# Kernel tuning notes

Hardware: AMD Instinct MI355X
Metric: run time of the kernel (lower is better)

Reference implementation:

```python
import jax, jax.numpy as jnp
import numpy as np

DIM = 512
DEPTH = 6
HEADS = 8
HD = DIM // HEADS          # head dim = 64
HALF = HD // 4             # rope half_dim = 16
MLP_H = int(DIM * 4.0)
TOKENS = [1, 4, 16, 64]    # CLS, S1, S2, S3
N = sum(TOKENS)            # 85
MAX_FREQ = 10.0
BATCH = 1024
LN_EPS = 1e-5


def _build_mask():
    # CLS sees CLS+S3; each scale sees CLS+itself (block-diagonal + CLS column)
    m = np.full((N, N), -np.inf, dtype=np.float32)
    cum = np.cumsum([0] + TOKENS)  # [0,1,5,21,85]
    m[0, 0] = 0.0
    m[0, cum[3]:cum[4]] = 0.0
    for i in range(1, 4):
        s, e = cum[i], cum[i + 1]
        m[s:e, 0] = 0.0
        m[s:e, s:e] = 0.0
    return jnp.asarray(m)

MASK = _build_mask()
FREQS = jnp.exp(jnp.arange(HALF, dtype=jnp.float32) * (-np.log(MAX_FREQ) / HALF))


def _layer_norm(x, g, b):
    mu = x.mean(-1, keepdims=True)
    var = ((x - mu) ** 2).mean(-1, keepdims=True)
    return (x - mu) * jax.lax.rsqrt(var + LN_EPS) * g + b


def _rope2d(t, coords):
    # t: [B,H,P,HD], coords: [P,2] in [0,1]^2
    ang_x = coords[:, 0:1] * FREQS[None, :] * (2.0 * jnp.pi)  # [P,HALF]
    ang_y = coords[:, 1:2] * FREQS[None, :] * (2.0 * jnp.pi)
    cx, sx = jnp.cos(ang_x), jnp.sin(ang_x)
    cy, sy = jnp.cos(ang_y), jnp.sin(ang_y)
    B, H, P, _ = t.shape
    t = t.reshape(B, H, P, 4, HALF)
    x0, x1, x2, x3 = t[..., 0, :], t[..., 1, :], t[..., 2, :], t[..., 3, :]
    r = jnp.stack([x0 * cx - x1 * sx,
                   x0 * sx + x1 * cx,
                   x2 * cy - x3 * sy,
                   x2 * sy + x3 * cy], axis=3)
    return r.reshape(B, H, P, HD)


def _rope_skip_cls(t, coords):
    return jnp.concatenate([t[:, :, :1], _rope2d(t[:, :, 1:], coords)], axis=2)


def _block(x, coords, p):
    (ln1g, ln1b, qkvw, qkvb, projw, projb,
     ln2g, ln2b, f1w, f1b, f2w, f2b) = p
    B, Nn, D = x.shape
    h = _layer_norm(x, ln1g, ln1b)
    qkv = h @ qkvw + qkvb                         # [B,N,3D]
    qkv = qkv.reshape(B, Nn, 3, HEADS, HD).transpose(2, 0, 3, 1, 4)
    q, k, v = qkv[0], qkv[1], qkv[2]              # [B,H,N,HD]
    q = _rope_skip_cls(q, coords)
    k = _rope_skip_cls(k, coords)
    attn = jnp.einsum('bhqd,bhkd->bhqk', q, k) * (HD ** -0.5) + MASK
    attn = jax.nn.softmax(attn, axis=-1)
    out = jnp.einsum('bhqk,bhkd->bhqd', attn, v)
    out = out.transpose(0, 2, 1, 3).reshape(B, Nn, D)
    x = x + (out @ projw + projb)
    h = _layer_norm(x, ln2g, ln2b)
    h = jax.nn.gelu(h @ f1w + f1b, approximate=False) @ f2w + f2b
    return x + h


def setup_inputs() -> dict:
    key = jax.random.key(0)
    ks = jax.random.split(key, 8)
    s = 0.02
    nrm = lambda k, shape: jax.random.normal(k, shape, jnp.float32) * s
    return dict(
        x=jax.random.normal(ks[0], (BATCH, N, DIM), jnp.float32),
        coords=jax.random.uniform(ks[1], (N - 1, 2), jnp.float32),
        ln1_g=jnp.ones((DEPTH, DIM), jnp.float32),
        ln1_b=jnp.zeros((DEPTH, DIM), jnp.float32),
        qkv_w=nrm(ks[2], (DEPTH, DIM, 3 * DIM)),
        qkv_b=jnp.zeros((DEPTH, 3 * DIM), jnp.float32),
        proj_w=nrm(ks[3], (DEPTH, DIM, DIM)),
        proj_b=jnp.zeros((DEPTH, DIM), jnp.float32),
        ln2_g=jnp.ones((DEPTH, DIM), jnp.float32),
        ln2_b=jnp.zeros((DEPTH, DIM), jnp.float32),
        fc1_w=nrm(ks[4], (DEPTH, DIM, MLP_H)),
        fc1_b=jnp.zeros((DEPTH, MLP_H), jnp.float32),
        fc2_w=nrm(ks[5], (DEPTH, MLP_H, DIM)),
        fc2_b=jnp.zeros((DEPTH, DIM), jnp.float32),
    )


def reference(x, coords, ln1_g, ln1_b, qkv_w, qkv_b, proj_w, proj_b,
              ln2_g, ln2_b, fc1_w, fc1_b, fc2_w, fc2_b):
    for i in range(DEPTH):
        x = _block(x, coords,
                   (ln1_g[i], ln1_b[i], qkv_w[i], qkv_b[i], proj_w[i], proj_b[i],
                    ln2_g[i], ln2_b[i], fc1_w[i], fc1_b[i], fc2_w[i], fc2_b[i]))
    return x
```

## Files before the change

kernel.cpp:

```cpp
#include <hip/hip_runtime.h>
#include <hip/hip_bf16.h>
#include <math.h>

#define DIMX 512
#define NTOK 85
#define BATCH 1024
#define M_ROWS (BATCH * NTOK)
#define MLP_H 2048
#define DEPTH 6

typedef __attribute__((ext_vector_type(8))) short short8;
typedef __attribute__((ext_vector_type(4))) float f32x4;

__device__ inline float bf2f(ushort u) {
    union { unsigned int i; float f; } v; v.i = ((unsigned int)u) << 16; return v.f;
}
__device__ inline ushort f2bf(float f) {
    __hip_bfloat16 h = __float2bfloat16(f);
    union { __hip_bfloat16 h; ushort u; } v; v.h = h; return v.u;
}
__device__ inline unsigned int pack2(float a, float b) {
    return (unsigned int)f2bf(a) | ((unsigned int)f2bf(b) << 16);
}
__device__ inline float gelu_fast(float v) {
    float u = 1.5957691f * fmaf(0.044715f * v, v * v, v);
    return v / (1.0f + __expf(-u));
}

__device__ inline void gload16(const ushort* g, ushort* lds) {
    __builtin_amdgcn_global_load_lds(
        (const __attribute__((address_space(1))) unsigned int*)g,
        (__attribute__((address_space(3))) unsigned int*)lds, 16, 0, 0);
}

__global__ __launch_bounds__(256) void transpose_bf16(const float* __restrict__ in,
                                                      ushort* __restrict__ out,
                                                      int K, int N) {
    __shared__ float tile[32][33];
    int n0 = blockIdx.x * 32, k0 = blockIdx.y * 32;
    int tx = threadIdx.x, ty = threadIdx.y;
    #pragma unroll
    for (int j = 0; j < 32; j += 8)
        tile[ty + j][tx] = in[(size_t)(k0 + ty + j) * N + n0 + tx];
    __syncthreads();
    #pragma unroll
    for (int j = 0; j < 32; j += 8)
        out[(size_t)(n0 + ty + j) * K + k0 + tx] = f2bf(tile[tx][ty + j]);
}

__global__ void rope_table(const float* __restrict__ coords, float* __restrict__ tab) {
    int t = blockIdx.x;
    int idx = threadIdx.x;
    float freq = expf(-(float)idx * (2.302585093f / 16.0f));
    float twopi = 6.283185307179586f;
    float ax = coords[t * 2 + 0] * freq * twopi;
    float ay = coords[t * 2 + 1] * freq * twopi;
    tab[t * 64 + idx]      = cosf(ax);
    tab[t * 64 + 16 + idx] = sinf(ax);
    tab[t * 64 + 32 + idx] = cosf(ay);
    tab[t * 64 + 48 + idx] = sinf(ay);
}

__global__ __launch_bounds__(256) void ln_kernel(const float* __restrict__ x,
                                                 const float* __restrict__ g,
                                                 const float* __restrict__ bta,
                                                 ushort* __restrict__ out) {
    int w = threadIdx.x >> 6, lane = threadIdx.x & 63;
    size_t row = (size_t)blockIdx.x * 4 + w;
    const float* xr = x + row * DIMX;
    int c = lane * 8;
    float4 v0 = *(const float4*)(xr + c);
    float4 v1 = *(const float4*)(xr + c + 4);
    float s = v0.x + v0.y + v0.z + v0.w + v1.x + v1.y + v1.z + v1.w;
    #pragma unroll
    for (int m = 32; m; m >>= 1) s += __shfl_xor(s, m);
    float mu = s * (1.0f / 512.0f);
    float d0 = v0.x - mu, d1 = v0.y - mu, d2 = v0.z - mu, d3 = v0.w - mu;
    float d4 = v1.x - mu, d5 = v1.y - mu, d6 = v1.z - mu, d7 = v1.w - mu;
    float q = d0*d0 + d1*d1 + d2*d2 + d3*d3 + d4*d4 + d5*d5 + d6*d6 + d7*d7;
    #pragma unroll
    for (int m = 32; m; m >>= 1) q += __shfl_xor(q, m);
    float rs = rsqrtf(q * (1.0f / 512.0f) + 1e-5f);
    float4 g0 = *(const float4*)(g + c), g1 = *(const float4*)(g + c + 4);
    float4 b0 = *(const float4*)(bta + c), b1 = *(const float4*)(bta + c + 4);
    uint4 o;
    o.x = pack2(d0 * rs * g0.x + b0.x, d1 * rs * g0.y + b0.y);
    o.y = pack2(d2 * rs * g0.z + b0.z, d3 * rs * g0.w + b0.w);
    o.z = pack2(d4 * rs * g1.x + b1.x, d5 * rs * g1.y + b1.y);
    o.w = pack2(d6 * rs * g1.z + b1.z, d7 * rs * g1.w + b1.w);
    *(uint4*)&out[row * DIMX + c] = o;
}

template <int EPI>
__global__ __launch_bounds__(256, 2) void gemm_wide(const ushort* __restrict__ A,
                                                    const ushort* __restrict__ Bt,
                                                    const float* __restrict__ bias,
                                                    float* __restrict__ outF,
                                                    ushort* __restrict__ outB,
                                                    int M, int N, int K,
                                                    const float* __restrict__ tab) {
    __shared__ ushort AsF[3 * 8192] __attribute__((aligned(16)));
    __shared__ ushort BsF[3 * 4096] __attribute__((aligned(16)));
    int tid = threadIdx.x;
    int w = tid >> 6, lane = tid & 63;
    int wm2 = (w >> 1) * 128;
    int wn = (w & 1) * 64;

    int nbx = gridDim.x;
    int nwg = nbx * gridDim.y;
    int orig = blockIdx.y * nbx + blockIdx.x;
    int q8 = nwg >> 3, r8 = nwg & 7;
    int xcd = orig & 7, loc = orig >> 3;
    int id = (xcd < r8) ? xcd * (q8 + 1) + loc : r8 * (q8 + 1) + (xcd - r8) * q8 + loc;
    int m0 = (id / nbx) * 256;
    int n0 = (id % nbx) * 128;

    int srow = tid >> 2;
    int scol = ((tid & 3) ^ ((srow >> 1) & 3)) * 8;
    int rA0 = m0 + srow;       if (rA0 >= M) rA0 = M - 1;
    int rA1 = m0 + 64 + srow;  if (rA1 >= M) rA1 = M - 1;
    int rA2 = m0 + 128 + srow; if (rA2 >= M) rA2 = M - 1;
    int rA3 = m0 + 192 + srow; if (rA3 >= M) rA3 = M - 1;
    const ushort* gA0 = A + (size_t)rA0 * K + scol;
    const ushort* gA1 = A + (size_t)rA1 * K + scol;
    const ushort* gA2 = A + (size_t)rA2 * K + scol;
    const ushort* gA3 = A + (size_t)rA3 * K + scol;
    const ushort* gB0 = Bt + (size_t)(n0 + srow) * K + scol;
    const ushort* gB1 = Bt + (size_t)(n0 + 64 + srow) * K + scol;
    int dwz = w * 512;
    int swA = 0, swB = 0;

#define STAGEW() do {                                                          \
        gload16(gA0, &AsF[swA + dwz]);                                         \
        gload16(gA1, &AsF[swA + 2048 + dwz]);                                  \
        gload16(gA2, &AsF[swA + 4096 + dwz]);                                  \
        gload16(gA3, &AsF[swA + 6144 + dwz]);                                  \
        gload16(gB0, &BsF[swB + dwz]);                                         \
        gload16(gB1, &BsF[swB + 2048 + dwz]);                                  \
        gA0 += 32; gA1 += 32; gA2 += 32; gA3 += 32; gB0 += 32; gB1 += 32;      \
        swA += 8192; if (swA == 24576) swA = 0;                                \
        swB += 4096; if (swB == 12288) swB = 0; } while (0)

    int l15 = lane & 15, lq = lane >> 4;
    int sw = (lq ^ ((l15 >> 1) & 3)) * 8;
    int aoff = (wm2 + l15) * 32 + sw;
    int boff = (wn + l15) * 32 + sw;
    int roffA = 0, roffB = 0;

    int NT = K >> 5;

    STAGEW(); STAGEW();

    f32x4 acc[8][4] = {};

    for (int t = 0; t < NT; ++t) {
        if (t < NT - 1) asm volatile("s_waitcnt vmcnt(6)" ::: "memory");
        else            asm volatile("s_waitcnt vmcnt(0)" ::: "memory");
        __builtin_amdgcn_s_barrier();
        short8 a[8], b[4];
        #pragma unroll
        for (int i = 0; i < 8; i++) a[i] = *(const short8*)&AsF[roffA + aoff + i * 512];
        #pragma unroll
        for (int j = 0; j < 4; j++) b[j] = *(const short8*)&BsF[roffB + boff + j * 512];
        if (t + 2 < NT) STAGEW();
        __builtin_amdgcn_s_setprio(1);
        #pragma unroll
        for (int i = 0; i < 8; i++)
            #pragma unroll
            for (int j = 0; j < 4; j++)
                acc[i][j] = __builtin_amdgcn_mfma_f32_16x16x32_bf16(a[i], b[j], acc[i][j], 0, 0, 0);
        __builtin_amdgcn_s_setprio(0);
        roffA += 8192; if (roffA == 24576) roffA = 0;
        roffB += 4096; if (roffB == 12288) roffB = 0;
    }
#undef STAGEW

    int cr = lq * 4;
    int cc = l15;
    if (EPI == 0) {
        bool ropeReg = (n0 + wn) < 1024;
        int gnb = n0 + wn + cc;
        float bb0 = bias[gnb], bb1 = bias[gnb + 16], bb2 = bias[gnb + 32], bb3 = bias[gnb + 48];
        #pragma unroll
        for (int i = 0; i < 8; i++) {
            #pragma unroll
            for (int rr = 0; rr < 4; rr++) {
                int gm = m0 + wm2 + i * 16 + cr + rr;
                if (gm >= M) continue;
                int n = gm % NTOK;
                float v0 = acc[i][0][rr] + bb0;
                float v1 = acc[i][1][rr] + bb1;
                float v2 = acc[i][2][rr] + bb2;
                float v3 = acc[i][3][rr] + bb3;
                if (ropeReg && n > 0) {
                    const float* tt = tab + (size_t)(n - 1) * 64 + cc;
                    float cx = tt[0], sx = tt[16], cy = tt[32], sy = tt[48];
                    float y0 = v0 * cx - v1 * sx;
                    float y1 = v0 * sx + v1 * cx;
                    float y2 = v2 * cy - v3 * sy;
                    float y3 = v2 * sy + v3 * cy;
                    v0 = y0; v1 = y1; v2 = y2; v3 = y3;
                }
                size_t o = (size_t)gm * N + gnb;
                outB[o]      = f2bf(v0);
                outB[o + 16] = f2bf(v1);
                outB[o + 32] = f2bf(v2);
                outB[o + 48] = f2bf(v3);
            }
        }
    } else {
        #pragma unroll
        for (int i = 0; i < 8; i++) {
            #pragma unroll
            for (int rr = 0; rr < 4; rr++) {
                int gm = m0 + wm2 + i * 16 + cr + rr;
                if (gm >= M) continue;
                #pragma unroll
                for (int j = 0; j < 4; j++) {
                    int gn = n0 + wn + j * 16 + cc;
                    float v = acc[i][j][rr] + bias[gn];
                    size_t o = (size_t)gm * N + gn;
                    if (EPI == 1) {
                        outF[o] = outF[o] + v;
                    } else {
                        outB[o] = f2bf(gelu_fast(v));
                    }
                }
            }
        }
    }
}

__global__ __launch_bounds__(384) void attn_kernel(const ushort* __restrict__ qkv,
                                                   ushort* __restrict__ out) {
    __shared__ ushort SU[13824] __attribute__((aligned(16)));
    __shared__ ushort Vt[6656]  __attribute__((aligned(16)));
    int bh = blockIdx.x;
    int b = bh >> 3, h = bh & 7;
    int tid = threadIdx.x;
    size_t base = (size_t)b * NTOK * 1536 + h * 64;

    for (int it = tid; it < 1536; it += 384) {
        int mat = (it >= 768) ? 1 : 0;
        int item = it - mat * 768;
        int n = item >> 3, g = item & 7;
        short8 v = {};
        if (n < NTOK)
            v = *(const short8*)&qkv[base + (size_t)n * 1536 + mat * 512 + g * 8];
        *(short8*)&SU[mat * 6912 + n * 72 + g * 8] = v;
    }
    for (int it = tid; it < 768; it += 384) {
        int n = it % 96;
        int d0 = (it / 96) * 8;
        short8 v = {};
        if (n < NTOK)
            v = *(const short8*)&qkv[base + (size_t)n * 1536 + 1024 + d0];
        #pragma unroll
        for (int j = 0; j < 8; j++)
            Vt[(d0 + j) * 104 + n] = (ushort)v[j];
    }
    __syncthreads();

    int wid = tid >> 6;
    int lane = tid & 63;
    int q = lane >> 4, c = lane & 15;
    int i0 = wid * 16;

    f32x4 acc[6] = {};
    #pragma unroll
    for (int kk = 0; kk < 2; kk++) {
        short8 aq = *(const short8*)&SU[(i0 + c) * 72 + kk * 32 + q * 8];
        #pragma unroll
        for (int t = 0; t < 6; t++) {
            short8 bk = *(const short8*)&SU[6912 + (t * 16 + c) * 72 + kk * 32 + q * 8];
            acc[t] = __builtin_amdgcn_mfma_f32_16x16x32_bf16(aq, bk, acc[t], 0, 0, 0);
        }
    }
    __syncthreads();

    #pragma unroll
    for (int r = 0; r < 4; r++) {
        int i = i0 + q * 4 + r;
        int si = (i == 0) ? 3 : (i < 5 ? 1 : (i < 21 ? 2 : 3));
        float vs[6];
        float m = -1e30f;
        #pragma unroll
        for (int t = 0; t < 6; t++) {
            int j = t * 16 + c;
            int sj = (j == 0) ? si : (j < 5 ? 1 : (j < 21 ? 2 : (j < NTOK ? 3 : -1)));
            float v = (sj == si) ? acc[t][r] * 0.125f : -1e30f;
            vs[t] = v;
            m = fmaxf(m, v);
        }
        #pragma unroll
        for (int mk = 8; mk; mk >>= 1) m = fmaxf(m, __shfl_xor(m, mk));
        float s = 0.f, ps[6];
        #pragma unroll
        for (int t = 0; t < 6; t++) { ps[t] = __expf(vs[t] - m); s += ps[t]; }
        #pragma unroll
        for (int mk = 8; mk; mk >>= 1) s += __shfl_xor(s, mk);
        float inv = 1.0f / s;
        #pragma unroll
        for (int t = 0; t < 6; t++)
            SU[i * 104 + t * 16 + c] = f2bf(ps[t] * inv);
    }
    __syncthreads();

    f32x4 o2[4] = {};
    #pragma unroll
    for (int kk = 0; kk < 3; kk++) {
        short8 ap = *(const short8*)&SU[(i0 + c) * 104 + kk * 32 + q * 8];
        #pragma unroll
        for (int nt = 0; nt < 4; nt++) {
            short8 bv = *(const short8*)&Vt[(nt * 16 + c) * 104 + kk * 32 + q * 8];
            o2[nt] = __builtin_amdgcn_mfma_f32_16x16x32_bf16(ap, bv, o2[nt], 0, 0, 0);
        }
    }
    size_t orow = (size_t)b * NTOK;
    #pragma unroll
    for (int nt = 0; nt < 4; nt++) {
        #pragma unroll
        for (int r = 0; r < 4; r++) {
            int i = i0 + q * 4 + r;
            if (i < NTOK)
                out[(orow + i) * DIMX + h * 64 + nt * 16 + c] = f2bf(o2[nt][r]);
        }
    }
}

extern "C" void kernel_launch(void* const* d_in, const int* in_sizes, int n_in,
                              void* d_out, int out_size, void* d_ws, size_t ws_size,
                              hipStream_t stream) {
    const float* x_in    = (const float*)d_in[0];
    const float* coords  = (const float*)d_in[1];
    const float* ln1_g   = (const float*)d_in[2];
    const float* ln1_b   = (const float*)d_in[3];
    const float* qkv_w   = (const float*)d_in[4];
    const float* qkv_b   = (const float*)d_in[5];
    const float* proj_w  = (const float*)d_in[6];
    const float* proj_b  = (const float*)d_in[7];
    const float* ln2_g   = (const float*)d_in[8];
    const float* ln2_b   = (const float*)d_in[9];
    const float* fc1_w   = (const float*)d_in[10];
    const float* fc1_b   = (const float*)d_in[11];
    const float* fc2_w   = (const float*)d_in[12];
    const float* fc2_b   = (const float*)d_in[13];

    char* ws = (char*)d_ws;
    size_t off = 0;
    auto alloc = [&](size_t bytes) -> void* {
        void* p = ws + off;
        off += (bytes + 255) & ~(size_t)255;
        return p;
    };
    auto asz = [](size_t b) { return (b + 255) & ~(size_t)255; };

    const size_t WPL = 512 * 1536 + 512 * 512 + 512 * 2048 + 2048 * 512;

    size_t fixed = asz(WPL * DEPTH * sizeof(ushort)) + asz(84 * 64 * sizeof(float));
    int Bc = 1024;
    while (Bc > 4) {
        size_t rc = (size_t)Bc * NTOK;
        size_t need = fixed + asz(rc * DIMX * sizeof(ushort)) + asz(rc * MLP_H * sizeof(ushort));
        if (need <= ws_size) break;
        Bc >>= 1;
    }
    size_t Rc = (size_t)Bc * NTOK;

    ushort* wt   = (ushort*)alloc(WPL * DEPTH * sizeof(ushort));
    float*  tab  = (float*)alloc(84 * 64 * sizeof(float));
    ushort* hbuf = (ushort*)alloc(Rc * DIMX * sizeof(ushort));
    ushort* big  = (ushort*)alloc(Rc * MLP_H * sizeof(ushort));

    hipMemcpyAsync(d_out, x_in, (size_t)M_ROWS * DIMX * sizeof(float),
                   hipMemcpyDeviceToDevice, stream);

    rope_table<<<84, 16, 0, stream>>>(coords, tab);

    dim3 tb(32, 8);
    for (int l = 0; l < DEPTH; l++) {
        ushort* wl = wt + (size_t)l * WPL;
        transpose_bf16<<<dim3(1536 / 32, 512 / 32), tb, 0, stream>>>(
            qkv_w + (size_t)l * 512 * 1536, wl, 512, 1536);
        transpose_bf16<<<dim3(512 / 32, 512 / 32), tb, 0, stream>>>(
            proj_w + (size_t)l * 512 * 512, wl + 786432, 512, 512);
        transpose_bf16<<<dim3(2048 / 32, 512 / 32), tb, 0, stream>>>(
            fc1_w + (size_t)l * 512 * 2048, wl + 1048576, 512, 2048);
        transpose_bf16<<<dim3(512 / 32, 2048 / 32), tb, 0, stream>>>(
            fc2_w + (size_t)l * 2048 * 512, wl + 2097152, 2048, 512);
    }

    int mt256 = (int)(Rc / 256);
    int lnblocks = (int)(Rc / 4);
    for (int c = 0; c < BATCH / Bc; c++) {
        float* xc = (float*)d_out + (size_t)c * Rc * DIMX;
        int Mc = (int)Rc;
        for (int l = 0; l < DEPTH; l++) {
            ushort* wl = wt + (size_t)l * WPL;
            ln_kernel<<<lnblocks, 256, 0, stream>>>(
                xc, ln1_g + l * 512, ln1_b + l * 512, hbuf);
            gemm_wide<0><<<dim3(1536 / 128, mt256), 256, 0, stream>>>(
                hbuf, wl, qkv_b + (size_t)l * 1536, nullptr, big, Mc, 1536, 512, tab);
            attn_kernel<<<Bc * 8, 384, 0, stream>>>(big, hbuf);
            gemm_wide<1><<<dim3(512 / 128, mt256), 256, 0, stream>>>(
                hbuf, wl + 786432, proj_b + (size_t)l * 512, xc, nullptr,
                Mc, 512, 512, nullptr);
            ln_kernel<<<lnblocks, 256, 0, stream>>>(
                xc, ln2_g + l * 512, ln2_b + l * 512, hbuf);
            gemm_wide<2><<<dim3(2048 / 128, mt256), 256, 0, stream>>>(
                hbuf, wl + 1048576, fc1_b + (size_t)l * 2048, nullptr, big,
                Mc, 2048, 512, nullptr);
            gemm_wide<1><<<dim3(512 / 128, mt256), 256, 0, stream>>>(
                big, wl + 2097152, fc2_b + (size_t)l * 512, xc, nullptr,
                Mc, 512, 2048, nullptr);
        }
    }
}
```

Baseline: 7.144 ms.

## Add barrier-free per-wave FC1 GEMM and drop initial residual copy

Adds a new gemm_nb kernel for the FC1+GELU GEMM. Each wave owns its own slice of LDS and stages its own 96x64 A/B subtiles with a double buffer, so no workgroup barriers are needed. Block tiles are 192x128, replacing the 256x128 shared-tile kernel. It also removes the device-to-device copy of x into the output by having layer 0 read x_in directly: the LN reads it, and the proj epilogue writes inF+v into out. This trades redundant global/L2 loads for the loss of barrier synchronisation, and saves one full-tensor copy.

```diff
diff --git a/kernel.cpp b/kernel.cpp
--- a/kernel.cpp
+++ b/kernel.cpp
@@ -95,6 +95,7 @@
 __global__ __launch_bounds__(256, 2) void gemm_wide(const ushort* __restrict__ A,
                                                     const ushort* __restrict__ Bt,
                                                     const float* __restrict__ bias,
+                                                    const float* __restrict__ inF,
                                                     float* __restrict__ outF,
                                                     ushort* __restrict__ outB,
                                                     int M, int N, int K,
@@ -148,7 +149,6 @@
     int roffA = 0, roffB = 0;
 
     int NT = K >> 5;
-
     STAGEW(); STAGEW();
 
     f32x4 acc[8][4] = {};
@@ -221,11 +221,110 @@
                     float v = acc[i][j][rr] + bias[gn];
                     size_t o = (size_t)gm * N + gn;
                     if (EPI == 1) {
-                        outF[o] = outF[o] + v;
+                        outF[o] = inF[o] + v;
                     } else {
                         outB[o] = f2bf(gelu_fast(v));
                     }
                 }
+            }
+        }
+    }
+}
+
+__global__ __launch_bounds__(256, 2) void gemm_nb(const ushort* __restrict__ A,
+                                                  const ushort* __restrict__ Bt,
+                                                  const float* __restrict__ bias,
+                                                  ushort* __restrict__ outB,
+                                                  int M, int N, int K) {
+    __shared__ ushort LDS[4 * 10240] __attribute__((aligned(16)));
+    int tid = threadIdx.x;
+    int w = tid >> 6, lane = tid & 63;
+    int wm = (w >> 1) * 96;
+    int wn = (w & 1) * 64;
+
+    int nbx = gridDim.x;
+    int nwg = nbx * gridDim.y;
+    int orig = blockIdx.y * nbx + blockIdx.x;
+    int q8 = nwg >> 3, r8 = nwg & 7;
+    int xcd = orig & 7, loc = orig >> 3;
+    int id = (xcd < r8) ? xcd * (q8 + 1) + loc : r8 * (q8 + 1) + (xcd - r8) * q8 + loc;
+    int m0 = (id / nbx) * 192;
+    int n0 = (id % nbx) * 128;
+
+    int srow = lane >> 2;
+    int scol = ((lane & 3) ^ ((srow >> 1) & 3)) * 8;
+    const ushort* pA[6];
+    const ushort* pB[4];
+    #pragma unroll
+    for (int i = 0; i < 6; i++) {
+        int r = m0 + wm + i * 16 + srow; if (r >= M) r = M - 1;
+        pA[i] = A + (size_t)r * K + scol;
+    }
+    #pragma unroll
+    for (int j = 0; j < 4; j++)
+        pB[j] = Bt + (size_t)(n0 + wn + j * 16 + srow) * K + scol;
+
+    ushort* LW = &LDS[w * 10240];
+
+#define STAGE_NB(T) do { int kc = (T) * 32, s = ((T) & 1);                     \
+        int da = s * 3072, db = 6144 + s * 2048;                               \
+        gload16(pA[0] + kc, &LW[da]);                                          \
+        gload16(pA[1] + kc, &LW[da + 512]);                                    \
+        gload16(pA[2] + kc, &LW[da + 1024]);                                   \
+        gload16(pA[3] + kc, &LW[da + 1536]);                                   \
+        gload16(pA[4] + kc, &LW[da + 2048]);                                   \
+        gload16(pA[5] + kc, &LW[da + 2560]);                                   \
+        gload16(pB[0] + kc, &LW[db]);                                          \
+        gload16(pB[1] + kc, &LW[db + 512]);                                    \
+        gload16(pB[2] + kc, &LW[db + 1024]);                                   \
+        gload16(pB[3] + kc, &LW[db + 1536]); } while (0)
+
+    int l15 = lane & 15, lq = lane >> 4;
+    int sw = (lq ^ ((l15 >> 1) & 3)) * 8;
+    int foff = l15 * 32 + sw;
+
+    int NT = K >> 5;
+    STAGE_NB(0);
+
+    f32x4 acc[6][4] = {};
+
+    for (int t = 0; t < NT; ++t) {
+        int ra = (t & 1) * 3072, rb = 6144 + (t & 1) * 2048;
+        if (t + 1 < NT) {
+            asm volatile("s_waitcnt lgkmcnt(0)" ::: "memory");
+            STAGE_NB(t + 1);
+            asm volatile("s_waitcnt vmcnt(10)" ::: "memory");
+        } else {
+            asm volatile("s_waitcnt vmcnt(0)" ::: "memory");
+        }
+        short8 a[6], b[4];
+        #pragma unroll
+        for (int i = 0; i < 6; i++) a[i] = *(const short8*)&LW[ra + foff + i * 512];
+        #pragma unroll
+        for (int j = 0; j < 4; j++) b[j] = *(const short8*)&LW[rb + foff + j * 512];
+        __builtin_amdgcn_s_setprio(1);
+        #pragma unroll
+        for (int i = 0; i < 6; i++)
+            #pragma unroll
+            for (int j = 0; j < 4; j++)
+                acc[i][j] = __builtin_amdgcn_mfma_f32_16x16x32_bf16(a[i], b[j], acc[i][j], 0, 0, 0);
+        __builtin_amdgcn_s_setprio(0);
+    }
+#undef STAGE_NB
+
+    int cr = lq * 4;
+    int cc = l15;
+    #pragma unroll
+    for (int i = 0; i < 6; i++) {
+        #pragma unroll
+        for (int rr = 0; rr < 4; rr++) {
+            int gm = m0 + wm + i * 16 + cr + rr;
+            if (gm >= M) continue;
+            #pragma unroll
+            for (int j = 0; j < 4; j++) {
+                int gn = n0 + wn + j * 16 + cc;
+                float v = acc[i][j][rr] + bias[gn];
+                outB[(size_t)gm * N + gn] = f2bf(gelu_fast(v));
             }
         }
     }
@@ -372,9 +471,6 @@
     ushort* hbuf = (ushort*)alloc(Rc * DIMX * sizeof(ushort));
     ushort* big  = (ushort*)alloc(Rc * MLP_H * sizeof(ushort));
 
-    hipMemcpyAsync(d_out, x_in, (size_t)M_ROWS * DIMX * sizeof(float),
-                   hipMemcpyDeviceToDevice, stream);
-
     rope_table<<<84, 16, 0, stream>>>(coords, tab);
 
     dim3 tb(32, 8);
@@ -391,27 +487,31 @@
     }
 
     int mt256 = (int)(Rc / 256);
+    int mt192 = (int)((Rc + 191) / 192);
     int lnblocks = (int)(Rc / 4);
     for (int c = 0; c < BATCH / Bc; c++) {
         float* xc = (float*)d_out + (size_t)c * Rc * DIMX;
+        const float* xin_c = x_in + (size_t)c * Rc * DIMX;
         int Mc = (int)Rc;
         for (int l = 0; l < DEPTH; l++) {
             ushort* wl = wt + (size_t)l * WPL;
+            const float* xsrc = (l == 0) ? xin_c : xc;
             ln_kernel<<<lnblocks, 256, 0, stream>>>(
-                xc, ln1_g + l * 512, ln1_b + l * 512, hbuf);
+                xsrc, ln1_g + l * 512, ln1_b + l * 512, hbuf);
             gemm_wide<0><<<dim3(1536 / 128, mt256), 256, 0, stream>>>(
-                hbuf, wl, qkv_b + (size_t)l * 1536, nullptr, big, Mc, 1536, 512, tab);
+                hbuf, wl, qkv_b + (size_t)l * 1536, nullptr, nullptr, big,
+                Mc, 1536, 512, tab);
             attn_kernel<<<Bc * 8, 384, 0, stream>>>(big, hbuf);
             gemm_wide<1><<<dim3(512 / 128, mt256), 256, 0, stream>>>(
-                hbuf, wl + 786432, proj_b + (size_t)l * 512, xc, nullptr,
+                hbuf, wl + 786432, proj_b + (size_t)l * 512, xsrc, xc, nullptr,
                 Mc, 512, 512, nullptr);
             ln_kernel<<<lnblocks, 256, 0, stream>>>(
                 xc, ln2_g + l * 512, ln2_b + l * 512, hbuf);
-            gemm_wide<2><<<dim3(2048 / 128, mt256), 256, 0, stream>>>(
-                hbuf, wl + 1048576, fc1_b + (size_t)l * 2048, nullptr, big,
-                Mc, 2048, 512, nullptr);
+            gemm_nb<<<dim3(2048 / 128, mt192), 256, 0, stream>>>(
+                hbuf, wl + 1048576, fc1_b + (size_t)l * 2048, big,
+                Mc, 2048, 512);
             gemm_wide<1><<<dim3(512 / 128, mt256), 256, 0, stream>>>(
-                big, wl + 2097152, fc2_b + (size_t)l * 512, xc, nullptr,
+                big, wl + 2097152, fc2_b + (size_t)l * 512, xc, xc, nullptr,
                 Mc, 512, 2048, nullptr);
         }
     }
```

Measured after the change: 7.209 ms. No clear change (+0.9%).

## Use 512-thread GEMM blocks with smaller per-wave tiles and drop input copy

Applied to the files above, without the earlier changes.

The GEMM now runs 8 waves per 256x128 tile instead of 4. Each wave holds a 64x64 accumulator rather than 128x64, and each thread issues fewer staging loads. This cuts register pressure and aims for more resident waves to hide latency, at the cost of less per-wave operand reuse. Separately, the initial device-to-device copy of x into the output is removed: layer 0 reads LayerNorm and the residual directly from the input, and the residual epilogue reads from a separate input pointer.

```diff
diff --git a/kernel.cpp b/kernel.cpp
--- a/kernel.cpp
+++ b/kernel.cpp
@@ -92,18 +92,19 @@
 }
 
 template <int EPI>
-__global__ __launch_bounds__(256, 2) void gemm_wide(const ushort* __restrict__ A,
-                                                    const ushort* __restrict__ Bt,
-                                                    const float* __restrict__ bias,
-                                                    float* __restrict__ outF,
-                                                    ushort* __restrict__ outB,
-                                                    int M, int N, int K,
-                                                    const float* __restrict__ tab) {
+__global__ __launch_bounds__(512, 4) void gemm_e(const ushort* __restrict__ A,
+                                                 const ushort* __restrict__ Bt,
+                                                 const float* __restrict__ bias,
+                                                 const float* __restrict__ inF,
+                                                 float* __restrict__ outF,
+                                                 ushort* __restrict__ outB,
+                                                 int M, int N, int K,
+                                                 const float* __restrict__ tab) {
     __shared__ ushort AsF[3 * 8192] __attribute__((aligned(16)));
     __shared__ ushort BsF[3 * 4096] __attribute__((aligned(16)));
     int tid = threadIdx.x;
     int w = tid >> 6, lane = tid & 63;
-    int wm2 = (w >> 1) * 128;
+    int wm = (w >> 1) * 64;
     int wn = (w & 1) * 64;
 
     int nbx = gridDim.x;
@@ -117,55 +118,46 @@
 
     int srow = tid >> 2;
     int scol = ((tid & 3) ^ ((srow >> 1) & 3)) * 8;
-    int rA0 = m0 + srow;       if (rA0 >= M) rA0 = M - 1;
-    int rA1 = m0 + 64 + srow;  if (rA1 >= M) rA1 = M - 1;
-    int rA2 = m0 + 128 + srow; if (rA2 >= M) rA2 = M - 1;
-    int rA3 = m0 + 192 + srow; if (rA3 >= M) rA3 = M - 1;
+    int rA0 = m0 + srow;        if (rA0 >= M) rA0 = M - 1;
+    int rA1 = m0 + 128 + srow;  if (rA1 >= M) rA1 = M - 1;
     const ushort* gA0 = A + (size_t)rA0 * K + scol;
     const ushort* gA1 = A + (size_t)rA1 * K + scol;
-    const ushort* gA2 = A + (size_t)rA2 * K + scol;
-    const ushort* gA3 = A + (size_t)rA3 * K + scol;
     const ushort* gB0 = Bt + (size_t)(n0 + srow) * K + scol;
-    const ushort* gB1 = Bt + (size_t)(n0 + 64 + srow) * K + scol;
     int dwz = w * 512;
     int swA = 0, swB = 0;
 
-#define STAGEW() do {                                                          \
+#define STAGEE() do {                                                          \
         gload16(gA0, &AsF[swA + dwz]);                                         \
-        gload16(gA1, &AsF[swA + 2048 + dwz]);                                  \
-        gload16(gA2, &AsF[swA + 4096 + dwz]);                                  \
-        gload16(gA3, &AsF[swA + 6144 + dwz]);                                  \
+        gload16(gA1, &AsF[swA + 4096 + dwz]);                                  \
         gload16(gB0, &BsF[swB + dwz]);                                         \
-        gload16(gB1, &BsF[swB + 2048 + dwz]);                                  \
-        gA0 += 32; gA1 += 32; gA2 += 32; gA3 += 32; gB0 += 32; gB1 += 32;      \
+        gA0 += 32; gA1 += 32; gB0 += 32;                                       \
         swA += 8192; if (swA == 24576) swA = 0;                                \
         swB += 4096; if (swB == 12288) swB = 0; } while (0)
 
     int l15 = lane & 15, lq = lane >> 4;
     int sw = (lq ^ ((l15 >> 1) & 3)) * 8;
-    int aoff = (wm2 + l15) * 32 + sw;
+    int aoff = (wm + l15) * 32 + sw;
     int boff = (wn + l15) * 32 + sw;
     int roffA = 0, roffB = 0;
 
     int NT = K >> 5;
-
-    STAGEW(); STAGEW();
-
-    f32x4 acc[8][4] = {};
+    STAGEE(); STAGEE();
+
+    f32x4 acc[4][4] = {};
 
     for (int t = 0; t < NT; ++t) {
-        if (t < NT - 1) asm volatile("s_waitcnt vmcnt(6)" ::: "memory");
+        if (t < NT - 1) asm volatile("s_waitcnt vmcnt(3)" ::: "memory");
         else            asm volatile("s_waitcnt vmcnt(0)" ::: "memory");
         __builtin_amdgcn_s_barrier();
-        short8 a[8], b[4];
-        #pragma unroll
-        for (int i = 0; i < 8; i++) a[i] = *(const short8*)&AsF[roffA + aoff + i * 512];
+        short8 a[4], b[4];
+        #pragma unroll
+        for (int i = 0; i < 4; i++) a[i] = *(const short8*)&AsF[roffA + aoff + i * 512];
         #pragma unroll
         for (int j = 0; j < 4; j++) b[j] = *(const short8*)&BsF[roffB + boff + j * 512];
-        if (t + 2 < NT) STAGEW();
+        if (t + 2 < NT) STAGEE();
         __builtin_amdgcn_s_setprio(1);
         #pragma unroll
-        for (int i = 0; i < 8; i++)
+        for (int i = 0; i < 4; i++)
             #pragma unroll
             for (int j = 0; j < 4; j++)
                 acc[i][j] = __builtin_amdgcn_mfma_f32_16x16x32_bf16(a[i], b[j], acc[i][j], 0, 0, 0);
@@ -173,7 +165,7 @@
         roffA += 8192; if (roffA == 24576) roffA = 0;
         roffB += 4096; if (roffB == 12288) roffB = 0;
     }
-#undef STAGEW
+#undef STAGEE
 
     int cr = lq * 4;
     int cc = l15;
@@ -182,10 +174,10 @@
         int gnb = n0 + wn + cc;
         float bb0 = bias[gnb], bb1 = bias[gnb + 16], bb2 = bias[gnb + 32], bb3 = bias[gnb + 48];
         #pragma unroll
-        for (int i = 0; i < 8; i++) {
+        for (int i = 0; i < 4; i++) {
             #pragma unroll
             for (int rr = 0; rr < 4; rr++) {
-                int gm = m0 + wm2 + i * 16 + cr + rr;
+                int gm = m0 + wm + i * 16 + cr + rr;
                 if (gm >= M) continue;
                 int n = gm % NTOK;
                 float v0 = acc[i][0][rr] + bb0;
@@ -210,10 +202,10 @@
         }
     } else {
         #pragma unroll
-        for (int i = 0; i < 8; i++) {
+        for (int i = 0; i < 4; i++) {
             #pragma unroll
             for (int rr = 0; rr < 4; rr++) {
-                int gm = m0 + wm2 + i * 16 + cr + rr;
+                int gm = m0 + wm + i * 16 + cr + rr;
                 if (gm >= M) continue;
                 #pragma unroll
                 for (int j = 0; j < 4; j++) {
@@ -221,7 +213,7 @@
                     float v = acc[i][j][rr] + bias[gn];
                     size_t o = (size_t)gm * N + gn;
                     if (EPI == 1) {
-                        outF[o] = outF[o] + v;
+                        outF[o] = inF[o] + v;
                     } else {
                         outB[o] = f2bf(gelu_fast(v));
                     }
@@ -372,9 +364,6 @@
     ushort* hbuf = (ushort*)alloc(Rc * DIMX * sizeof(ushort));
     ushort* big  = (ushort*)alloc(Rc * MLP_H * sizeof(ushort));
 
-    hipMemcpyAsync(d_out, x_in, (size_t)M_ROWS * DIMX * sizeof(float),
-                   hipMemcpyDeviceToDevice, stream);
-
     rope_table<<<84, 16, 0, stream>>>(coords, tab);
 
     dim3 tb(32, 8);
@@ -394,24 +383,27 @@
     int lnblocks = (int)(Rc / 4);
     for (int c = 0; c < BATCH / Bc; c++) {
         float* xc = (float*)d_out + (size_t)c * Rc * DIMX;
+        const float* xin_c = x_in + (size_t)c * Rc * DIMX;
         int Mc = (int)Rc;
         for (int l = 0; l < DEPTH; l++) {
             ushort* wl = wt + (size_t)l * WPL;
+            const float* xsrc = (l == 0) ? xin_c : xc;
             ln_kernel<<<lnblocks, 256, 0, stream>>>(
-                xc, ln1_g + l * 512, ln1_b + l * 512, hbuf);
-            gemm_wide<0><<<dim3(1536 / 128, mt256), 256, 0, stream>>>(
-                hbuf, wl, qkv_b + (size_t)l * 1536, nullptr, big, Mc, 1536, 512, tab);
+                xsrc, ln1_g + l * 512, ln1_b + l * 512, hbuf);
+            gemm_e<0><<<dim3(1536 / 128, mt256), 512, 0, stream>>>(
+                hbuf, wl, qkv_b + (size_t)l * 1536, nullptr, nullptr, big,
+                Mc, 1536, 512, tab);
             attn_kernel<<<Bc * 8, 384, 0, stream>>>(big, hbuf);
-            gemm_wide<1><<<dim3(512 / 128, mt256), 256, 0, stream>>>(
-                hbuf, wl + 786432, proj_b + (size_t)l * 512, xc, nullptr,
+            gemm_e<1><<<dim3(512 / 128, mt256), 512, 0, stream>>>(
+                hbuf, wl + 786432, proj_b + (size_t)l * 512, xsrc, xc, nullptr,
                 Mc, 512, 512, nullptr);
             ln_kernel<<<lnblocks, 256, 0, stream>>>(
                 xc, ln2_g + l * 512, ln2_b + l * 512, hbuf);
-            gemm_wide<2><<<dim3(2048 / 128, mt256), 256, 0, stream>>>(
-                hbuf, wl + 1048576, fc1_b + (size_t)l * 2048, nullptr, big,
-                Mc, 2048, 512, nullptr);
-            gemm_wide<1><<<dim3(512 / 128, mt256), 256, 0, stream>>>(
-                big, wl + 2097152, fc2_b + (size_t)l * 512, xc, nullptr,
+            gemm_e<2><<<dim3(2048 / 128, mt256), 512, 0, stream>>>(
+                hbuf, wl + 1048576, fc1_b + (size_t)l * 2048, nullptr, nullptr,
+                big, Mc, 2048, 512, nullptr);
+            gemm_e<1><<<dim3(512 / 128, mt256), 512, 0, stream>>>(
+                big, wl + 2097152, fc2_b + (size_t)l * 512, xc, xc, nullptr,
                 Mc, 512, 2048, nullptr);
         }
     }
```

Result: faster. 6.671 ms (median of 3 runs) (-6.6%).
